# Optimization experiments

Hardware: AMD Instinct MI355X
Metric: run time of the kernel (lower is better)

## Reference

```python
import jax, jax.numpy as jnp
import numpy as np

B, S, D = 4, 1024, 1024
H = 16
HD = D // H  # head_dim = 64


def setup_inputs() -> dict:
    key = jax.random.key(0)
    k1, k2, k3 = jax.random.split(key, 3)
    x = jax.random.normal(k1, (B, S, D), dtype=jnp.float32)
    # qkv_proj: Linear(input_dim, 3*embed_dim), stored as (in, out) for x @ W
    scale = 1.0 / np.sqrt(D)
    W_qkv = jax.random.uniform(k2, (D, 3 * D), dtype=jnp.float32, minval=-scale, maxval=scale)
    b_qkv = jax.random.uniform(k3, (3 * D,), dtype=jnp.float32, minval=-scale, maxval=scale)
    return {"x": x, "W_qkv": W_qkv, "b_qkv": b_qkv}


def reference(x, W_qkv, b_qkv):
    b, s, _ = x.shape
    qkv = x @ W_qkv + b_qkv                       # [B,S,3D]
    qkv = qkv.reshape(b, s, H, 3 * HD)            # [B,S,H,3*hd]
    qkv = qkv.transpose(0, 2, 1, 3)               # [B,H,S,3*hd]
    q, k, v = jnp.split(qkv, 3, axis=-1)          # each [B,H,S,hd]
    scores = jnp.einsum('bhqd,bhkd->bhqk', q, k) / jnp.sqrt(jnp.float32(HD))
    attn = jax.nn.softmax(scores, axis=-1)        # [B,H,S,S]
    out = jnp.einsum('bhqk,bhkd->bhqd', attn, v)  # [B,H,S,hd]
    values = out.transpose(0, 2, 1, 3).reshape(b, s, H * HD)  # [B,S,D]
    return values
```

## Files before the change

kernel.cpp:

```cpp
#include <hip/hip_runtime.h>
#include <hip/hip_bf16.h>
#include <stdint.h>

#define BATCH 4
#define SEQ 1024
#define DMODEL 1024
#define NH 16
#define HD 64

typedef __attribute__((ext_vector_type(8))) short short8;
typedef __attribute__((ext_vector_type(4))) float f32x4;
typedef __attribute__((ext_vector_type(4))) unsigned short ushort4v;

__device__ __forceinline__ unsigned short f2bf(float f) {
    union { float f; uint32_t u; } v; v.f = f;
    uint32_t r = v.u + 0x7fff + ((v.u >> 16) & 1);
    return (unsigned short)(r >> 16);
}

__device__ __forceinline__ uint32_t pack2bf(float lo, float hi) {
    return (uint32_t)f2bf(lo) | ((uint32_t)f2bf(hi) << 16);
}

__global__ __launch_bounds__(256) void prep_kernel(const float* __restrict__ x,
                                                   const float* __restrict__ W,
                                                   unsigned short* __restrict__ xb,
                                                   unsigned short* __restrict__ Wt) {
    __shared__ float tile[32][33];
    int bid = blockIdx.x;
    if (bid < 2048) {
        int t = bid * 256 + threadIdx.x;
        const float4* p = (const float4*)x + (size_t)t * 2;
        float4 a = p[0], b = p[1];
        short8 o;
        o[0] = (short)f2bf(a.x); o[1] = (short)f2bf(a.y);
        o[2] = (short)f2bf(a.z); o[3] = (short)f2bf(a.w);
        o[4] = (short)f2bf(b.x); o[5] = (short)f2bf(b.y);
        o[6] = (short)f2bf(b.z); o[7] = (short)f2bf(b.w);
        *((short8*)xb + t) = o;
    } else {
        int r = bid - 2048;
        int nb = (r % 96) * 32;
        int kb = (r / 96) * 32;
        int tx = threadIdx.x & 31;
        int ty = threadIdx.x >> 5;
#pragma unroll
        for (int i = 0; i < 4; i++) {
            int k = kb + ty + i * 8;
            tile[ty + i * 8][tx] = W[(size_t)k * 3072 + nb + tx];
        }
        __syncthreads();
#pragma unroll
        for (int i = 0; i < 4; i++) {
            int n = nb + ty + i * 8;
            Wt[(size_t)n * 1024 + kb + tx] = f2bf(tile[tx][ty + i * 8]);
        }
    }
}

#define BM 128
#define BN 128
#define BKK 64

__global__ __launch_bounds__(256, 3) void qkv_gemm_kernel(
    const unsigned short* __restrict__ xb,
    const unsigned short* __restrict__ wt,
    const float* __restrict__ bias,
    unsigned short* __restrict__ Qb,
    unsigned short* __restrict__ Kb,
    unsigned short* __restrict__ VbT)
{
    __shared__ __align__(16) unsigned short As[BM][64];
    __shared__ __align__(16) unsigned short Bs[BN][64];
    int tid = threadIdx.x;
    int wave = tid >> 6, lane = tid & 63;
    int quad = lane >> 4, l16 = lane & 15;
    int wm = wave >> 1, wn = wave & 1;
    int m0 = blockIdx.x * BM;
    int n0 = blockIdx.y * BN;

    int grow = lane >> 3;
    int gcol = ((lane & 7) ^ grow) << 3;
    const unsigned short* gA = xb + (size_t)(m0 + wave * 32 + grow) * 1024 + gcol;
    const unsigned short* gB = wt + (size_t)(n0 + wave * 32 + grow) * 1024 + gcol;
    unsigned short* ldsA = &As[wave * 32][0] + lane * 8;
    unsigned short* ldsB = &Bs[wave * 32][0] + lane * 8;
    int sw = l16 & 7;

    short8 areg[4], breg[4];
#pragma unroll
    for (int i = 0; i < 4; i++) {
        areg[i] = *(const short8*)(gA + (size_t)i * 8 * 1024);
        breg[i] = *(const short8*)(gB + (size_t)i * 8 * 1024);
    }

    f32x4 acc[4][4] = {};
    for (int k0 = 0; k0 < 1024; k0 += BKK) {
        __syncthreads();
#pragma unroll
        for (int i = 0; i < 4; i++) {
            *(short8*)(ldsA + i * 512) = areg[i];
            *(short8*)(ldsB + i * 512) = breg[i];
        }
        __syncthreads();
        if (k0 + BKK < 1024) {
#pragma unroll
            for (int i = 0; i < 4; i++) {
                areg[i] = *(const short8*)(gA + (size_t)i * 8 * 1024 + k0 + BKK);
                breg[i] = *(const short8*)(gB + (size_t)i * 8 * 1024 + k0 + BKK);
            }
        }
#pragma unroll
        for (int kk = 0; kk < BKK; kk += 32) {
            int kb = kk >> 3;
            short8 af[4], bf[4];
#pragma unroll
            for (int t = 0; t < 4; t++) {
                int ar = wm * 64 + t * 16 + l16;
                af[t] = *(const short8*)&As[ar][((kb + quad) ^ sw) << 3];
            }
#pragma unroll
            for (int t = 0; t < 4; t++) {
                int br = wn * 64 + t * 16 + l16;
                bf[t] = *(const short8*)&Bs[br][((kb + quad) ^ sw) << 3];
            }
#pragma unroll
            for (int mt = 0; mt < 4; mt++)
#pragma unroll
                for (int nt = 0; nt < 4; nt++)
                    acc[mt][nt] = __builtin_amdgcn_mfma_f32_16x16x32_bf16(
                        af[mt], bf[nt], acc[mt][nt], 0, 0, 0);
        }
    }
#pragma unroll
    for (int nt = 0; nt < 4; nt++) {
        int n = n0 + wn * 64 + nt * 16 + l16;
        int h = n / 192;
        int c = n - h * 192;
        int which = c >> 6;
        int d = c & 63;
        float bv = bias[n];
        if (which == 2) {
#pragma unroll
            for (int mt = 0; mt < 4; mt++) {
                int m = m0 + wm * 64 + mt * 16 + quad * 4;
                int b = m >> 10, s = m & 1023;
                ushort4v o;
                o[0] = f2bf(acc[mt][nt][0] + bv);
                o[1] = f2bf(acc[mt][nt][1] + bv);
                o[2] = f2bf(acc[mt][nt][2] + bv);
                o[3] = f2bf(acc[mt][nt][3] + bv);
                *(ushort4v*)&VbT[((size_t)((b * 16 + h) * 64 + d)) * 1024 + s] = o;
            }
        } else {
            unsigned short* dst = (which == 0) ? Qb : Kb;
            float sc = (which == 0) ? 0.125f : 1.0f;
#pragma unroll
            for (int mt = 0; mt < 4; mt++) {
#pragma unroll
                for (int r = 0; r < 4; r++) {
                    int m = m0 + wm * 64 + mt * 16 + quad * 4 + r;
                    int b = m >> 10, s = m & 1023;
                    dst[((size_t)((b * 16 + h) * 1024 + s)) * 64 + d] = f2bf((acc[mt][nt][r] + bv) * sc);
                }
            }
        }
    }
}

#define BQ 128
#define BKV 128

__global__ __launch_bounds__(256, 3) void attn_kernel(
    const unsigned short* __restrict__ Qb,
    const unsigned short* __restrict__ Kb,
    const unsigned short* __restrict__ VbT,
    float* __restrict__ out)
{
    __shared__ unsigned short Qs[BQ][64];
    __shared__ unsigned short Ks[BKV][64];
    __shared__ unsigned short Vts[HD][128];

    int tid = threadIdx.x;
    int wave = tid >> 6, lane = tid & 63;
    int quad = lane >> 4, l16 = lane & 15;

    int id = blockIdx.x;
    int xcd = id & 7, rest = id >> 3;
    int qt = rest & 7, grp = rest >> 3;
    int bh = grp * 8 + xcd;
    int q0 = qt * BQ;

    const unsigned short* Qp = Qb + (size_t)bh * SEQ * HD;
    const unsigned short* Kp = Kb + (size_t)bh * SEQ * HD;
    const unsigned short* Vp = VbT + (size_t)bh * HD * SEQ;

    int f_q = (l16 & 3) | (((l16 >> 3) & 1) << 2);
    int f_k = (l16 & 3) | (((l16 >> 2) & 1) << 2);
    int f_v = l16 & 7;
    int rbase = ((l16 >> 2) << 3) | (l16 & 3);

#pragma unroll
    for (int i = 0; i < 4; i++) {
        int idx = i * 256 + tid;
        int row = idx >> 3, pb = idx & 7;
        int fr = (row & 3) | (((row >> 3) & 1) << 2);
        int lb = pb ^ fr;
        *(short8*)&Qs[row][pb * 8] = *(const short8*)&Qp[(size_t)(q0 + row) * HD + lb * 8];
    }

    short8 kreg[4], vreg[4];
    auto load_tile = [&](int kt) {
#pragma unroll
        for (int i = 0; i < 4; i++) {
            int idx = i * 256 + tid;
            int krow = idx >> 3, kpb = idx & 7;
            int klb = kpb ^ ((krow & 3) | (((krow >> 3) & 1) << 2));
            kreg[i] = *(const short8*)&Kp[(size_t)(kt + krow) * HD + klb * 8];
            int vrow = idx >> 4, vpb = idx & 15;
            int vlb = vpb ^ (vrow & 7);
            vreg[i] = *(const short8*)&Vp[(size_t)vrow * SEQ + kt + vlb * 8];
        }
    };
    load_tile(0);

    f32x4 oacc[2][4] = {};
    float lsum[2] = {0.f, 0.f};

    for (int kt = 0; kt < SEQ; kt += BKV) {
        __syncthreads();
#pragma unroll
        for (int i = 0; i < 4; i++) {
            int idx = i * 256 + tid;
            int krow = idx >> 3, kpb = idx & 7;
            *(short8*)&Ks[krow][kpb * 8] = kreg[i];
            int vrow = idx >> 4, vpb = idx & 15;
            *(short8*)&Vts[vrow][vpb * 8] = vreg[i];
        }
        __syncthreads();
        if (kt + BKV < SEQ) load_tile(kt + BKV);

        short8 qf[2][2];
#pragma unroll
        for (int kc = 0; kc < 2; kc++)
#pragma unroll
            for (int g = 0; g < 2; g++)
                qf[g][kc] = *(const short8*)&Qs[wave * 32 + g * 16 + l16][((kc * 4 + quad) ^ f_q) * 8];

#pragma unroll
        for (int c = 0; c < 4; c++) {
            int base = rbase + (c << 5);
            f32x4 s0[2] = {}, s1[2] = {};
#pragma unroll
            for (int kc = 0; kc < 2; kc++) {
                short8 kf0 = *(const short8*)&Ks[base][((kc * 4 + quad) ^ f_k) * 8];
                short8 kf1 = *(const short8*)&Ks[base + 4][((kc * 4 + quad) ^ f_k) * 8];
#pragma unroll
                for (int g = 0; g < 2; g++) {
                    s0[g] = __builtin_amdgcn_mfma_f32_16x16x32_bf16(kf0, qf[g][kc], s0[g], 0, 0, 0);
                    s1[g] = __builtin_amdgcn_mfma_f32_16x16x32_bf16(kf1, qf[g][kc], s1[g], 0, 0, 0);
                }
            }
            short8 vf[4];
#pragma unroll
            for (int nt = 0; nt < 4; nt++)
                vf[nt] = *(const short8*)&Vts[nt * 16 + l16][(((c << 2) + quad) ^ f_v) * 8];
#pragma unroll
            for (int g = 0; g < 2; g++) {
                float p0 = __expf(s0[g][0]);
                float p1 = __expf(s0[g][1]);
                float p2 = __expf(s0[g][2]);
                float p3 = __expf(s0[g][3]);
                float p4 = __expf(s1[g][0]);
                float p5 = __expf(s1[g][1]);
                float p6 = __expf(s1[g][2]);
                float p7 = __expf(s1[g][3]);
                lsum[g] += ((p0 + p1) + (p2 + p3)) + ((p4 + p5) + (p6 + p7));
                union { uint32_t w[4]; short8 s; } pf;
                pf.w[0] = pack2bf(p0, p1);
                pf.w[1] = pack2bf(p2, p3);
                pf.w[2] = pack2bf(p4, p5);
                pf.w[3] = pack2bf(p6, p7);
#pragma unroll
                for (int nt = 0; nt < 4; nt++)
                    oacc[g][nt] = __builtin_amdgcn_mfma_f32_16x16x32_bf16(vf[nt], pf.s, oacc[g][nt], 0, 0, 0);
            }
        }
    }

#pragma unroll
    for (int g = 0; g < 2; g++) {
        lsum[g] += __shfl_xor(lsum[g], 16, 64);
        lsum[g] += __shfl_xor(lsum[g], 32, 64);
    }

    int b = bh >> 4, h = bh & 15;
#pragma unroll
    for (int g = 0; g < 2; g++) {
        float inv = 1.f / lsum[g];
        int s = q0 + wave * 32 + g * 16 + l16;
#pragma unroll
        for (int nt = 0; nt < 4; nt++) {
            float4 o;
            o.x = oacc[g][nt][0] * inv;
            o.y = oacc[g][nt][1] * inv;
            o.z = oacc[g][nt][2] * inv;
            o.w = oacc[g][nt][3] * inv;
            *(float4*)&out[(size_t)(b * SEQ + s) * DMODEL + h * HD + nt * 16 + quad * 4] = o;
        }
    }
}

extern "C" void kernel_launch(void* const* d_in, const int* in_sizes, int n_in,
                              void* d_out, int out_size, void* d_ws, size_t ws_size,
                              hipStream_t stream) {
    const float* x    = (const float*)d_in[0];
    const float* W    = (const float*)d_in[1];
    const float* bias = (const float*)d_in[2];
    float* out = (float*)d_out;
    char* ws = (char*)d_ws;

    unsigned short* xb  = (unsigned short*)(ws);
    unsigned short* wt  = (unsigned short*)(ws + 8388608);
    unsigned short* Qb  = (unsigned short*)(ws + 14680064);
    unsigned short* Kb  = (unsigned short*)(ws + 23068672);
    unsigned short* VbT = (unsigned short*)(ws + 31457280);

    prep_kernel<<<5120, 256, 0, stream>>>(x, W, xb, wt);
    dim3 gg(32, 24);
    qkv_gemm_kernel<<<gg, 256, 0, stream>>>(xb, wt, bias, Qb, Kb, VbT);
    attn_kernel<<<512, 256, 0, stream>>>(Qb, Kb, VbT, out);
}
```

Before: 161.0 us.

## Split attention KV dimension across waves with LDS reduction and exp2 softmax

The attention kernel now uses 64-query tiles, with each wave owning a 32-key slice of each KV tile instead of a slice of queries. Partial outputs and row sums are combined through a shared-memory tree reduction at the end, and the grid doubles to 1024 blocks. Q fragments are kept in registers loaded straight from global memory, and the register prefetch of the next K/V tile is dropped. The log2(e) factor is folded into the Q scale so the kernel can use the hardware exp2, and bf16 packing switches to the HIP intrinsic. The intent is more blocks for occupancy and fewer K/V LDS reads per MFMA. The cost is extra reduction traffic and syncs, loss of load/compute overlap, and occupancy now bounded at 2 blocks.

```diff
diff --git a/kernel.cpp b/kernel.cpp
--- a/kernel.cpp
+++ b/kernel.cpp
@@ -19,7 +19,9 @@
 }
 
 __device__ __forceinline__ uint32_t pack2bf(float lo, float hi) {
-    return (uint32_t)f2bf(lo) | ((uint32_t)f2bf(hi) << 16);
+    union { __hip_bfloat162 h; uint32_t u; } cv;
+    cv.h = __float22bfloat162_rn(make_float2(lo, hi));
+    return cv.u;
 }
 
 __global__ __launch_bounds__(256) void prep_kernel(const float* __restrict__ x,
@@ -61,6 +63,7 @@
 #define BM 128
 #define BN 128
 #define BKK 64
+#define QSCALE 0.18033688011112042f
 
 __global__ __launch_bounds__(256, 3) void qkv_gemm_kernel(
     const unsigned short* __restrict__ xb,
@@ -154,7 +157,7 @@
             }
         } else {
             unsigned short* dst = (which == 0) ? Qb : Kb;
-            float sc = (which == 0) ? 0.125f : 1.0f;
+            float sc = (which == 0) ? QSCALE : 1.0f;
 #pragma unroll
             for (int mt = 0; mt < 4; mt++) {
 #pragma unroll
@@ -168,18 +171,20 @@
     }
 }
 
-#define BQ 128
+#define BQ 64
 #define BKV 128
 
-__global__ __launch_bounds__(256, 3) void attn_kernel(
+__global__ __launch_bounds__(256, 2) void attn_kernel(
     const unsigned short* __restrict__ Qb,
     const unsigned short* __restrict__ Kb,
     const unsigned short* __restrict__ VbT,
     float* __restrict__ out)
 {
-    __shared__ unsigned short Qs[BQ][64];
-    __shared__ unsigned short Ks[BKV][64];
-    __shared__ unsigned short Vts[HD][128];
+    __shared__ __align__(16) char smem[32768];
+    __shared__ float lbuf[4][4][16];
+    unsigned short (*Ks)[64]  = (unsigned short(*)[64])smem;
+    unsigned short (*Vts)[128] = (unsigned short(*)[128])(smem + 16384);
+    float* red = (float*)smem;
 
     int tid = threadIdx.x;
     int wave = tid >> 6, lane = tid & 63;
@@ -187,7 +192,7 @@
 
     int id = blockIdx.x;
     int xcd = id & 7, rest = id >> 3;
-    int qt = rest & 7, grp = rest >> 3;
+    int qt = rest & 15, grp = rest >> 4;
     int bh = grp * 8 + xcd;
     int q0 = qt * BQ;
 
@@ -195,118 +200,135 @@
     const unsigned short* Kp = Kb + (size_t)bh * SEQ * HD;
     const unsigned short* Vp = VbT + (size_t)bh * HD * SEQ;
 
-    int f_q = (l16 & 3) | (((l16 >> 3) & 1) << 2);
     int f_k = (l16 & 3) | (((l16 >> 2) & 1) << 2);
     int f_v = l16 & 7;
-    int rbase = ((l16 >> 2) << 3) | (l16 & 3);
-
-#pragma unroll
-    for (int i = 0; i < 4; i++) {
-        int idx = i * 256 + tid;
-        int row = idx >> 3, pb = idx & 7;
-        int fr = (row & 3) | (((row >> 3) & 1) << 2);
-        int lb = pb ^ fr;
-        *(short8*)&Qs[row][pb * 8] = *(const short8*)&Qp[(size_t)(q0 + row) * HD + lb * 8];
-    }
-
-    short8 kreg[4], vreg[4];
-    auto load_tile = [&](int kt) {
+    int krow0 = (wave << 5) + ((l16 >> 2) << 3) + (l16 & 3);
+
+    short8 qf[4][2];
+#pragma unroll
+    for (int g = 0; g < 4; g++)
+#pragma unroll
+        for (int kc = 0; kc < 2; kc++)
+            qf[g][kc] = *(const short8*)&Qp[(size_t)(q0 + g * 16 + l16) * HD + kc * 32 + quad * 8];
+
+    f32x4 oacc[4][4] = {};
+    float lsum[4] = {0.f, 0.f, 0.f, 0.f};
+
+    for (int kt = 0; kt < SEQ; kt += BKV) {
+        __syncthreads();
 #pragma unroll
         for (int i = 0; i < 4; i++) {
             int idx = i * 256 + tid;
             int krow = idx >> 3, kpb = idx & 7;
             int klb = kpb ^ ((krow & 3) | (((krow >> 3) & 1) << 2));
-            kreg[i] = *(const short8*)&Kp[(size_t)(kt + krow) * HD + klb * 8];
+            *(short8*)&Ks[krow][kpb * 8] = *(const short8*)&Kp[(size_t)(kt + krow) * HD + klb * 8];
             int vrow = idx >> 4, vpb = idx & 15;
             int vlb = vpb ^ (vrow & 7);
-            vreg[i] = *(const short8*)&Vp[(size_t)vrow * SEQ + kt + vlb * 8];
-        }
-    };
-    load_tile(0);
-
-    f32x4 oacc[2][4] = {};
-    float lsum[2] = {0.f, 0.f};
-
-    for (int kt = 0; kt < SEQ; kt += BKV) {
-        __syncthreads();
-#pragma unroll
-        for (int i = 0; i < 4; i++) {
-            int idx = i * 256 + tid;
-            int krow = idx >> 3, kpb = idx & 7;
-            *(short8*)&Ks[krow][kpb * 8] = kreg[i];
-            int vrow = idx >> 4, vpb = idx & 15;
-            *(short8*)&Vts[vrow][vpb * 8] = vreg[i];
-        }
-        __syncthreads();
-        if (kt + BKV < SEQ) load_tile(kt + BKV);
-
-        short8 qf[2][2];
-#pragma unroll
-        for (int kc = 0; kc < 2; kc++)
-#pragma unroll
-            for (int g = 0; g < 2; g++)
-                qf[g][kc] = *(const short8*)&Qs[wave * 32 + g * 16 + l16][((kc * 4 + quad) ^ f_q) * 8];
-
-#pragma unroll
-        for (int c = 0; c < 4; c++) {
-            int base = rbase + (c << 5);
-            f32x4 s0[2] = {}, s1[2] = {};
+            *(short8*)&Vts[vrow][vpb * 8] = *(const short8*)&Vp[(size_t)vrow * SEQ + kt + vlb * 8];
+        }
+        __syncthreads();
+
+        short8 kf[2][2], vf[4];
+#pragma unroll
+        for (int t = 0; t < 2; t++)
+#pragma unroll
+            for (int kc = 0; kc < 2; kc++)
+                kf[t][kc] = *(const short8*)&Ks[krow0 + t * 4][(((kc << 2) + quad) ^ f_k) * 8];
+#pragma unroll
+        for (int nt = 0; nt < 4; nt++)
+            vf[nt] = *(const short8*)&Vts[nt * 16 + l16][(((wave << 2) + quad) ^ f_v) * 8];
+
+#pragma unroll
+        for (int g = 0; g < 4; g++) {
+            f32x4 s0 = {}, s1 = {};
 #pragma unroll
             for (int kc = 0; kc < 2; kc++) {
-                short8 kf0 = *(const short8*)&Ks[base][((kc * 4 + quad) ^ f_k) * 8];
-                short8 kf1 = *(const short8*)&Ks[base + 4][((kc * 4 + quad) ^ f_k) * 8];
-#pragma unroll
-                for (int g = 0; g < 2; g++) {
-                    s0[g] = __builtin_amdgcn_mfma_f32_16x16x32_bf16(kf0, qf[g][kc], s0[g], 0, 0, 0);
-                    s1[g] = __builtin_amdgcn_mfma_f32_16x16x32_bf16(kf1, qf[g][kc], s1[g], 0, 0, 0);
-                }
-            }
-            short8 vf[4];
+                s0 = __builtin_amdgcn_mfma_f32_16x16x32_bf16(kf[0][kc], qf[g][kc], s0, 0, 0, 0);
+                s1 = __builtin_amdgcn_mfma_f32_16x16x32_bf16(kf[1][kc], qf[g][kc], s1, 0, 0, 0);
+            }
+            float p0 = __builtin_amdgcn_exp2f(s0[0]);
+            float p1 = __builtin_amdgcn_exp2f(s0[1]);
+            float p2 = __builtin_amdgcn_exp2f(s0[2]);
+            float p3 = __builtin_amdgcn_exp2f(s0[3]);
+            float p4 = __builtin_amdgcn_exp2f(s1[0]);
+            float p5 = __builtin_amdgcn_exp2f(s1[1]);
+            float p6 = __builtin_amdgcn_exp2f(s1[2]);
+            float p7 = __builtin_amdgcn_exp2f(s1[3]);
+            lsum[g] += ((p0 + p1) + (p2 + p3)) + ((p4 + p5) + (p6 + p7));
+            union { uint32_t w[4]; short8 s; } pf;
+            pf.w[0] = pack2bf(p0, p1);
+            pf.w[1] = pack2bf(p2, p3);
+            pf.w[2] = pack2bf(p4, p5);
+            pf.w[3] = pack2bf(p6, p7);
 #pragma unroll
             for (int nt = 0; nt < 4; nt++)
-                vf[nt] = *(const short8*)&Vts[nt * 16 + l16][(((c << 2) + quad) ^ f_v) * 8];
-#pragma unroll
-            for (int g = 0; g < 2; g++) {
-                float p0 = __expf(s0[g][0]);
-                float p1 = __expf(s0[g][1]);
-                float p2 = __expf(s0[g][2]);
-                float p3 = __expf(s0[g][3]);
-                float p4 = __expf(s1[g][0]);
-                float p5 = __expf(s1[g][1]);
-                float p6 = __expf(s1[g][2]);
-                float p7 = __expf(s1[g][3]);
-                lsum[g] += ((p0 + p1) + (p2 + p3)) + ((p4 + p5) + (p6 + p7));
-                union { uint32_t w[4]; short8 s; } pf;
-                pf.w[0] = pack2bf(p0, p1);
-                pf.w[1] = pack2bf(p2, p3);
-                pf.w[2] = pack2bf(p4, p5);
-                pf.w[3] = pack2bf(p6, p7);
-#pragma unroll
-                for (int nt = 0; nt < 4; nt++)
-                    oacc[g][nt] = __builtin_amdgcn_mfma_f32_16x16x32_bf16(vf[nt], pf.s, oacc[g][nt], 0, 0, 0);
-            }
-        }
-    }
-
-#pragma unroll
-    for (int g = 0; g < 2; g++) {
+                oacc[g][nt] = __builtin_amdgcn_mfma_f32_16x16x32_bf16(vf[nt], pf.s, oacc[g][nt], 0, 0, 0);
+        }
+    }
+
+#pragma unroll
+    for (int g = 0; g < 4; g++) {
         lsum[g] += __shfl_xor(lsum[g], 16, 64);
         lsum[g] += __shfl_xor(lsum[g], 32, 64);
     }
-
-    int b = bh >> 4, h = bh & 15;
-#pragma unroll
-    for (int g = 0; g < 2; g++) {
-        float inv = 1.f / lsum[g];
-        int s = q0 + wave * 32 + g * 16 + l16;
-#pragma unroll
-        for (int nt = 0; nt < 4; nt++) {
-            float4 o;
-            o.x = oacc[g][nt][0] * inv;
-            o.y = oacc[g][nt][1] * inv;
-            o.z = oacc[g][nt][2] * inv;
-            o.w = oacc[g][nt][3] * inv;
-            *(float4*)&out[(size_t)(b * SEQ + s) * DMODEL + h * HD + nt * 16 + quad * 4] = o;
+    int off = quad * 16 + l16;
+    __syncthreads();
+    if (wave >= 2) {
+        float* r = red + (wave - 2) * 4096;
+#pragma unroll
+        for (int g = 0; g < 4; g++)
+#pragma unroll
+            for (int nt = 0; nt < 4; nt++)
+#pragma unroll
+                for (int rr = 0; rr < 4; rr++)
+                    r[((g * 4 + nt) * 4 + rr) * 64 + off] = oacc[g][nt][rr];
+        if (quad == 0)
+#pragma unroll
+            for (int g = 0; g < 4; g++) lbuf[wave][g][l16] = lsum[g];
+    }
+    __syncthreads();
+    if (wave < 2) {
+        float* r = red + wave * 4096;
+#pragma unroll
+        for (int g = 0; g < 4; g++) {
+#pragma unroll
+            for (int nt = 0; nt < 4; nt++)
+#pragma unroll
+                for (int rr = 0; rr < 4; rr++)
+                    oacc[g][nt][rr] += r[((g * 4 + nt) * 4 + rr) * 64 + off];
+            lsum[g] += lbuf[wave + 2][g][l16];
+        }
+    }
+    __syncthreads();
+    if (wave == 1) {
+#pragma unroll
+        for (int g = 0; g < 4; g++)
+#pragma unroll
+            for (int nt = 0; nt < 4; nt++)
+#pragma unroll
+                for (int rr = 0; rr < 4; rr++)
+                    red[((g * 4 + nt) * 4 + rr) * 64 + off] = oacc[g][nt][rr];
+        if (quad == 0)
+#pragma unroll
+            for (int g = 0; g < 4; g++) lbuf[1][g][l16] = lsum[g];
+    }
+    __syncthreads();
+    if (wave == 0) {
+        int b = bh >> 4, h = bh & 15;
+#pragma unroll
+        for (int g = 0; g < 4; g++) {
+            float l = lsum[g] + lbuf[1][g][l16];
+            float inv = 1.f / l;
+            int s = q0 + g * 16 + l16;
+#pragma unroll
+            for (int nt = 0; nt < 4; nt++) {
+                float4 o;
+                o.x = (oacc[g][nt][0] + red[((g * 4 + nt) * 4 + 0) * 64 + off]) * inv;
+                o.y = (oacc[g][nt][1] + red[((g * 4 + nt) * 4 + 1) * 64 + off]) * inv;
+                o.z = (oacc[g][nt][2] + red[((g * 4 + nt) * 4 + 2) * 64 + off]) * inv;
+                o.w = (oacc[g][nt][3] + red[((g * 4 + nt) * 4 + 3) * 64 + off]) * inv;
+                *(float4*)&out[(size_t)(b * SEQ + s) * DMODEL + h * HD + nt * 16 + quad * 4] = o;
+            }
         }
     }
 }
@@ -329,5 +351,5 @@
     prep_kernel<<<5120, 256, 0, stream>>>(x, W, xb, wt);
     dim3 gg(32, 24);
     qkv_gemm_kernel<<<gg, 256, 0, stream>>>(xb, wt, bias, Qb, Kb, VbT);
-    attn_kernel<<<512, 256, 0, stream>>>(Qb, Kb, VbT, out);
-}
+    attn_kernel<<<1024, 256, 0, stream>>>(Qb, Kb, VbT, out);
+}
```

Result: faster. 145.4 us (-9.7%).
